# Performance work log

Measured on AMD Instinct MI355X. Metric: run time of the kernel, lower is better.

Reference implementation:

```python
import jax, jax.numpy as jnp
import numpy as np

SHIFTS = [1, 3, 5, 7]
C = 16  # in_channels // 4
# -1 neighbor offsets for tmp1..tmp8 (dy, dx) in units of the dilation
OFFSETS = [(-1, -1), (-1, 0), (-1, 1), (0, 1), (1, 1), (1, 0), (1, -1), (0, -1)]


def setup_inputs() -> dict:
    key = jax.random.key(0)
    ks = jax.random.split(key, 32)
    d = {}
    d['cen'] = jax.random.normal(ks[0], (8, 64, 256, 256), jnp.float32)
    d['mas'] = jax.random.normal(ks[1], (8, 1, 256, 256), jnp.float32)
    d['in_conv_w'] = jax.random.normal(ks[2], (16, 64), jnp.float32) * 0.1
    d['in_conv_b'] = jax.random.normal(ks[3], (16,), jnp.float32) * 0.1
    for i, s in enumerate(SHIFTS):
        d[f'dw_w{s}'] = jax.random.normal(ks[4 + 2 * i], (16, 1, s, s), jnp.float32) * 0.1
        d[f'dw_b{s}'] = jax.random.normal(ks[5 + 2 * i], (16,), jnp.float32) * 0.1
    d['l1_w'] = jax.random.normal(ks[12], (4, 16, 4), jnp.float32) * 0.1
    d['l1_b'] = jax.random.normal(ks[13], (4, 16), jnp.float32) * 0.1
    d['l2_w'] = jax.random.normal(ks[14], (4, 16, 8), jnp.float32) * 0.1
    d['l2_b'] = jax.random.normal(ks[15], (4, 16), jnp.float32) * 0.1
    d['base_w'] = jax.random.normal(ks[16], (16, 4), jnp.float32) * 0.1
    d['bn_scale'] = jnp.ones((16,), jnp.float32)
    d['bn_bias'] = jnp.zeros((16,), jnp.float32)
    d['final_w'] = jax.random.normal(ks[17], (1, 16), jnp.float32) * 0.1
    d['final_b'] = jax.random.normal(ks[18], (1,), jnp.float32) * 0.1
    return d


def _dw_conv(x, w, b, pad):
    # depthwise conv, groups == channels
    y = jax.lax.conv_general_dilated(
        x, w, window_strides=(1, 1), padding=[(pad, pad), (pad, pad)],
        dimension_numbers=('NCHW', 'OIHW', 'NCHW'), feature_group_count=x.shape[1])
    return y + b[None, :, None, None]


def _shifted(x, dy, dx, d):
    # zero-padded shift: out(y,x) = in(y+dy, x+dx)
    H, W = x.shape[2], x.shape[3]
    p = jnp.pad(x, ((0, 0), (0, 0), (d, d), (d, d)))
    return p[:, :, d + dy:d + dy + H, d + dx:d + dx + W]


def _circ_shift(x, dw_w, dw_b, w1, b1, w2, b2, shift):
    x = _dw_conv(x, dw_w, dw_b, shift // 2)
    # tmp_k = x - x shifted by the k-th neighbor offset (dilation = shift)
    T = [x - _shifted(x, dy * shift, dx * shift, shift) for dy, dx in OFFSETS]
    # paired sums: S[k] = tmp_{k+1} + tmp_{k+5} (S repeats with period 4)
    S = [T[k] + T[k + 4] for k in range(4)]
    outs = []
    for k in range(8):  # fixed small structural loop
        feats = jnp.stack([S[(k + 1) % 4], S[(k + 3) % 4], S[(k + 2) % 4],
                           2.0 * T[(k + 4) % 8]], axis=2)  # (B,C,4,H,W)
        # grouped 1x1 conv (groups=C, 4C->C) == per-channel contraction over feature axis
        o = jnp.einsum('bcfhw,cf->bchw', feats, w1) + b1[None, :, None, None]
        outs.append(o * T[k])
    O = jnp.sort(jnp.stack(outs, axis=2), axis=2)  # (B,C,8,H,W) sorted over branch axis
    return jnp.einsum('bcfhw,cf->bchw', O, w2) + b2[None, :, None, None]


def reference(cen, mas, in_conv_w, in_conv_b, dw_w1, dw_b1, dw_w3, dw_b3,
              dw_w5, dw_b5, dw_w7, dw_b7, l1_w, l1_b, l2_w, l2_b,
              base_w, bn_scale, bn_bias, final_w, final_b):
    # in_conv: 1x1, in_channels -> C
    x = jnp.einsum('bihw,oi->bohw', cen, in_conv_w) + in_conv_b[None, :, None, None]
    dws = [(dw_w1, dw_b1), (dw_w3, dw_b3), (dw_w5, dw_b5), (dw_w7, dw_b7)]
    branches = [
        _circ_shift(x, dws[i][0], dws[i][1], l1_w[i], l1_b[i], l2_w[i], l2_b[i], SHIFTS[i])
        for i in range(len(SHIFTS))
    ]
    A = jnp.sort(jnp.stack(branches, axis=2), axis=2)  # (B,C,4,H,W)
    # out_conv: grouped 1x1 BaseConv (conv no-bias + BN(affine) + SiLU), then 1x1 -> 1, sigmoid
    y = jnp.einsum('bcfhw,cf->bchw', A, base_w)
    y = jax.nn.silu(y * bn_scale[None, :, None, None] + bn_bias[None, :, None, None])
    y = jnp.einsum('bchw,oc->bohw', y, final_w) + final_b[None, :, None, None]
    return jax.nn.sigmoid(y)
```

## Files before the change

kernel.cpp:

```cpp
#include <hip/hip_runtime.h>
#include <hip/hip_fp16.h>
#include <math.h>

#define HW 65536

typedef float v2f __attribute__((ext_vector_type(2), aligned(8)));
typedef _Float16 h2 __attribute__((ext_vector_type(2)));

__device__ __forceinline__ h2 uh(unsigned u) { return __builtin_bit_cast(h2, u); }
__device__ __forceinline__ unsigned hu(h2 v) { return __builtin_bit_cast(unsigned, v); }

#define CEH(a, b) { h2 _t = __builtin_elementwise_min(a, b); \
                    b = __builtin_elementwise_max(a, b); a = _t; }

__device__ __forceinline__ void sort8_h2(h2* v) {
    CEH(v[0], v[1]); CEH(v[2], v[3]); CEH(v[4], v[5]); CEH(v[6], v[7]);
    CEH(v[0], v[2]); CEH(v[1], v[3]); CEH(v[4], v[6]); CEH(v[5], v[7]);
    CEH(v[1], v[2]); CEH(v[5], v[6]); CEH(v[0], v[4]); CEH(v[3], v[7]);
    CEH(v[1], v[5]); CEH(v[2], v[6]);
    CEH(v[1], v[4]); CEH(v[3], v[6]);
    CEH(v[2], v[4]); CEH(v[3], v[5]);
    CEH(v[3], v[4]);
}
__device__ __forceinline__ void sort4_h2(h2* v) {
    CEH(v[0], v[1]); CEH(v[2], v[3]); CEH(v[0], v[2]); CEH(v[1], v[3]); CEH(v[1], v[2]);
}

__global__ __launch_bounds__(256) void k_pack(const float* __restrict__ l1w,
                                              const float* __restrict__ l1b,
                                              const float* __restrict__ l2w,
                                              const float* __restrict__ l2b,
                                              const float* __restrict__ bw,
                                              const float* __restrict__ dw_w1,
                                              const float* __restrict__ dw_b1,
                                              const float* __restrict__ dw_w3,
                                              const float* __restrict__ dw_b3,
                                              const float* __restrict__ dw_w5,
                                              const float* __restrict__ dw_b5,
                                              const float* __restrict__ dw_w7,
                                              const float* __restrict__ dw_b7,
                                              unsigned* __restrict__ wtab) {
    for (int t = threadIdx.x; t < 3584; t += 256) {
        float v = 0.f;
        if (t < 1024) {
            int c = t >> 6, i = (t >> 4) & 3, j = t & 15;
            if (j < 3)        v = l1w[i * 64 + c * 4 + j];
            else if (j == 3)  v = 2.f * l1w[i * 64 + c * 4 + 3];
            else if (j == 4)  v = l1b[i * 16 + c];
            else if (j < 13)  v = l2w[i * 128 + c * 8 + (j - 5)];
            else if (j == 13) v = l2b[i * 16 + c];
        } else if (t < 1088) {
            v = bw[t - 1024];
        } else if (t >= 2048) {
            int c = (t - 2048) / 96, j = (t - 2048) - c * 96;
            if (j < 49)       v = dw_w7[c * 49 + j];
            else if (j < 74)  v = dw_w5[c * 25 + (j - 49)];
            else if (j < 83)  v = dw_w3[c * 9 + (j - 74)];
            else if (j == 83) v = dw_w1[c];
            else if (j == 84) v = dw_b1[c];
            else if (j == 85) v = dw_b3[c];
            else if (j == 86) v = dw_b5[c];
            else if (j == 87) v = dw_b7[c];
        }
        unsigned hs = (unsigned)__half_as_ushort(__float2half(v));
        wtab[t] = hs * 0x10001u;
    }
}

__global__ __launch_bounds__(256, 4) void k_inconv(const float* __restrict__ cen,
                                                   const float* __restrict__ w,
                                                   const float* __restrict__ bias,
                                                   __half* __restrict__ xh) {
    __shared__ float wl[1040];
    int tid = threadIdx.x;
    for (int t = tid; t < 1024; t += 256) wl[t] = w[(t & 15) * 64 + (t >> 4)];
    if (tid < 16) wl[1024 + tid] = bias[tid];
    __syncthreads();

    int q  = blockIdx.x * 256 + tid;
    int b_ = q >> 14;
    int hw = (q & 16383) * 4;
    const float* src = cen + (size_t)(b_ * 64) * HW + hw;

    float4 acc[16];
#pragma unroll
    for (int o = 0; o < 16; o++) { float bv = wl[1024 + o]; acc[o] = make_float4(bv, bv, bv, bv); }

#pragma unroll 4
    for (int i = 0; i < 64; i++) {
        float4 xv = *(const float4*)(src + (size_t)i * HW);
        const float4* wq = (const float4*)&wl[i * 16];
#pragma unroll
        for (int g = 0; g < 4; g++) {
            float4 f = wq[g];
            acc[g * 4 + 0].x += xv.x * f.x; acc[g * 4 + 0].y += xv.y * f.x;
            acc[g * 4 + 0].z += xv.z * f.x; acc[g * 4 + 0].w += xv.w * f.x;
            acc[g * 4 + 1].x += xv.x * f.y; acc[g * 4 + 1].y += xv.y * f.y;
            acc[g * 4 + 1].z += xv.z * f.y; acc[g * 4 + 1].w += xv.w * f.y;
            acc[g * 4 + 2].x += xv.x * f.z; acc[g * 4 + 2].y += xv.y * f.z;
            acc[g * 4 + 2].z += xv.z * f.z; acc[g * 4 + 2].w += xv.w * f.z;
            acc[g * 4 + 3].x += xv.x * f.w; acc[g * 4 + 3].y += xv.y * f.w;
            acc[g * 4 + 3].z += xv.z * f.w; acc[g * 4 + 3].w += xv.w * f.w;
        }
    }
    __half* dst = xh + (size_t)(b_ * 16) * HW + hw;
#pragma unroll
    for (int o = 0; o < 16; o++) {
        uint2 pk;
        pk.x = __builtin_bit_cast(unsigned, __floats2half2_rn(acc[o].x, acc[o].y));
        pk.y = __builtin_bit_cast(unsigned, __floats2half2_rn(acc[o].z, acc[o].w));
        *(uint2*)(dst + (size_t)o * HW) = pk;
    }
}

__global__ __launch_bounds__(512, 4) void k_fused(const __half* __restrict__ xh,
    const unsigned* __restrict__ wtab,
    const float* __restrict__ bns, const float* __restrict__ bnb,
    __half* __restrict__ y16) {

    const int by  = blockIdx.y;
    const int c   = by & 15;
    const int ty0 = (blockIdx.x >> 3) * 32;
    const int tx0 = (blockIdx.x & 7) * 32;
    const int tid = threadIdx.x;

    __shared__ unsigned lxh[52 * 27];
    __shared__ __align__(16) unsigned convt[4 * 46 * 24];

    {
        const unsigned* xp32 = (const unsigned*)(xh + (size_t)by * HW);
        for (int t = tid; t < 52 * 26; t += 512) {
            int r = t / 26, j = t - r * 26;
            int gy = ty0 - 10 + r, gp = tx0 - 10 + 2 * j;
            unsigned v = 0;
            if ((unsigned)gy < 256u && (unsigned)gp < 256u)
                v = xp32[(gy << 7) + (gp >> 1)];
            lxh[r * 27 + j] = v;
        }
    }
    __syncthreads();

    {
        const unsigned* dwc = wtab + 2048 + c * 96;
        for (int u = tid; u < 46 * 23; u += 512) {
            int row = u / 23;
            int d0  = u - row * 23;
            int pc0 = d0 * 2;
            h2 acc7 = {0, 0}, acc5 = {0, 0}, acc3 = {0, 0}, acc1 = {0, 0};
#pragma unroll
            for (int a = 0; a < 7; a++) {
                const unsigned* rp = lxh + (row + a) * 27 + d0;
                unsigned q0 = rp[0], q1 = rp[1], q2 = rp[2], q3 = rp[3], q4 = rp[4];
                unsigned p1u = (q0 >> 16) | (q1 << 16);
                unsigned p3u = (q1 >> 16) | (q2 << 16);
                unsigned p5u = (q2 >> 16) | (q3 << 16);
                unsigned p7u = (q3 >> 16) | (q4 << 16);
                h2 P[8] = {uh(q0), uh(p1u), uh(q1), uh(p3u),
                           uh(q2), uh(p5u), uh(q3), uh(p7u)};
#pragma unroll
                for (int b = 0; b < 7; b++)
                    acc7 = P[b] * uh(dwc[a * 7 + b]) + acc7;
                if (a >= 1 && a <= 5) {
#pragma unroll
                    for (int b = 0; b < 5; b++)
                        acc5 = P[1 + b] * uh(dwc[49 + (a - 1) * 5 + b]) + acc5;
                }
                if (a >= 2 && a <= 4) {
#pragma unroll
                    for (int b = 0; b < 3; b++)
                        acc3 = P[2 + b] * uh(dwc[74 + (a - 2) * 3 + b]) + acc3;
                }
                if (a == 3)
                    acc1 = P[3] * uh(dwc[83]);
            }
            int iy = ty0 - 7 + row, ix = tx0 - 7 + pc0;
            bool rin = (unsigned)iy < 256u;
            unsigned msk = (rin && (unsigned)ix < 256u ? 0x0000FFFFu : 0u)
                         | (rin && (unsigned)(ix + 1) < 256u ? 0xFFFF0000u : 0u);
            int o = row * 24 + d0;
            convt[o]        = hu(acc1 + uh(dwc[84])) & msk;
            convt[o + 1104] = hu(acc3 + uh(dwc[85])) & msk;
            convt[o + 2208] = hu(acc5 + uh(dwc[86])) & msk;
            convt[o + 3312] = hu(acc7 + uh(dwc[87])) & msk;
        }
    }
    __syncthreads();

    const int py  = tid >> 4;
    const int pxp = tid & 15;

    h2 bh[4];
#pragma unroll
    for (int i = 0; i < 4; i++) {
        const int s = 1 + 2 * i;
        const unsigned* pl = convt + i * 1104;
        const int q    = pxp + (7 - s) / 2;
        const int topb = (py + 7 - s) * 24 + q;
        const int midb = (py + 7) * 24 + q;
        const int botb = (py + 7 + s) * 24 + q;

        unsigned tt[8], tm[8], tb[8];
#pragma unroll
        for (int k = 0; k <= s; k++) {
            tt[k] = pl[topb + k];
            tm[k] = pl[midb + k];
            tb[k] = pl[botb + k];
        }
        const int m = s >> 1;
        h2 n0  = uh(tt[0]);
        h2 n1  = uh((tt[m] >> 16) | (tt[m + 1] << 16));
        h2 n2  = uh(tt[s]);
        h2 n7  = uh(tm[0]);
        h2 ctr = uh((tm[m] >> 16) | (tm[m + 1] << 16));
        h2 n3  = uh(tm[s]);
        h2 n6  = uh(tb[0]);
        h2 n5  = uh((tb[m] >> 16) | (tb[m + 1] << 16));
        h2 n4  = uh(tb[s]);

        h2 T[8];
        T[0] = ctr - n0; T[1] = ctr - n1; T[2] = ctr - n2; T[3] = ctr - n3;
        T[4] = ctr - n4; T[5] = ctr - n5; T[6] = ctr - n6; T[7] = ctr - n7;
        h2 S[4];
#pragma unroll
        for (int k = 0; k < 4; k++) S[k] = T[k] + T[k + 4];

        const unsigned* wt = wtab + ((c << 2) + i) * 16;
        h2 w10 = uh(wt[0]), w11 = uh(wt[1]), w12 = uh(wt[2]);
        h2 w13x2 = uh(wt[3]), bb1 = uh(wt[4]);

        h2 R[4];
#pragma unroll
        for (int mm = 0; mm < 4; mm++) {
            h2 r = S[(mm + 2) & 3] * w12 + bb1;
            r = S[(mm + 3) & 3] * w11 + r;
            r = S[(mm + 1) & 3] * w10 + r;
            R[mm] = r;
        }
        h2 h8[8];
#pragma unroll
        for (int k = 0; k < 8; k++)
            h8[k] = (T[(k + 4) & 7] * w13x2 + R[k & 3]) * T[k];
        sort8_h2(h8);

        h2 acc = uh(wt[13]);
#pragma unroll
        for (int k = 0; k < 8; k++) acc += h8[k] * uh(wt[5 + k]);
        bh[i] = acc;
    }
    sort4_h2(bh);
    h2 yv = bh[0] * uh(wtab[1024 + (c << 2)]);
#pragma unroll
    for (int k = 1; k < 4; k++) yv = bh[k] * uh(wtab[1024 + (c << 2) + k]) + yv;

    const float bsc = bns[c], bbi = bnb[c];
    float zx = fmaf((float)yv.x, bsc, bbi);
    float zy = fmaf((float)yv.y, bsc, bbi);
    float sx = zx / (1.f + __expf(-zx));
    float sy = zy / (1.f + __expf(-zy));
    *(__half2*)&y16[(size_t)by * HW + (ty0 + py) * 256 + tx0 + 2 * pxp] =
        __floats2half2_rn(sx, sy);
}

__global__ __launch_bounds__(256) void k_final(const __half* __restrict__ y16,
                                               const float* __restrict__ fw,
                                               const float* __restrict__ fb,
                                               float* __restrict__ out) {
    long t  = (long)blockIdx.x * 256 + threadIdx.x;
    long p0 = t * 2;
    int  b  = (int)(p0 >> 16);
    int  hw = (int)(p0 & 65535);

    float accx = fb[0], accy = fb[0];
#pragma unroll
    for (int cc = 0; cc < 16; cc++) {
        __half2 h = *(const __half2*)(y16 + (size_t)(b * 16 + cc) * HW + hw);
        float2 v = __half22float2(h);
        float wv = fw[cc];
        accx = fmaf(v.x, wv, accx);
        accy = fmaf(v.y, wv, accy);
    }
    float2 r;
    r.x = 1.f / (1.f + __expf(-accx));
    r.y = 1.f / (1.f + __expf(-accy));
    *(float2*)(out + p0) = r;
}

extern "C" void kernel_launch(void* const* d_in, const int* in_sizes, int n_in,
                              void* d_out, int out_size, void* d_ws, size_t ws_size,
                              hipStream_t stream) {
    (void)in_sizes; (void)n_in; (void)out_size; (void)ws_size;
    const float* cen   = (const float*)d_in[0];
    const float* in_w  = (const float*)d_in[2];
    const float* in_b  = (const float*)d_in[3];
    const float* dw_w1 = (const float*)d_in[4];
    const float* dw_b1 = (const float*)d_in[5];
    const float* dw_w3 = (const float*)d_in[6];
    const float* dw_b3 = (const float*)d_in[7];
    const float* dw_w5 = (const float*)d_in[8];
    const float* dw_b5 = (const float*)d_in[9];
    const float* dw_w7 = (const float*)d_in[10];
    const float* dw_b7 = (const float*)d_in[11];
    const float* l1w   = (const float*)d_in[12];
    const float* l1b   = (const float*)d_in[13];
    const float* l2w   = (const float*)d_in[14];
    const float* l2b   = (const float*)d_in[15];
    const float* bw    = (const float*)d_in[16];
    const float* bns   = (const float*)d_in[17];
    const float* bnb   = (const float*)d_in[18];
    const float* fw    = (const float*)d_in[19];
    const float* fb    = (const float*)d_in[20];

    __half*   xh   = (__half*)d_ws;
    unsigned* wtab = (unsigned*)((char*)d_ws + (size_t)16777216);
    __half*   y16  = (__half*)((char*)d_ws + (size_t)16777216 + 16384);
    float*    out  = (float*)d_out;

    k_pack<<<1, 256, 0, stream>>>(l1w, l1b, l2w, l2b, bw,
                                  dw_w1, dw_b1, dw_w3, dw_b3,
                                  dw_w5, dw_b5, dw_w7, dw_b7, wtab);
    k_inconv<<<512, 256, 0, stream>>>(cen, in_w, in_b, xh);
    k_fused<<<dim3(64, 128), 512, 0, stream>>>(xh, wtab, bns, bnb, y16);
    k_final<<<1024, 256, 0, stream>>>(y16, fw, fb, out);
}
```

Measured before the change: 359.1 us.

## Enlarge fused tile to 64x64 with 1024 threads; narrow inconv per-thread width

The fused kernel moves from 32x32 to 64x64 spatial tiles with 1024 threads, each thread computing two output rows. This cuts the halo overhead of the staged input and the depthwise-conv intermediates relative to useful output. Shared-memory strides change to 43 and 40 words, and the conv loop no longer loads an unused fifth word. The in_conv kernel now handles 2 pixels per thread instead of 4 and launches twice as many blocks for more parallelism. The cost is higher LDS use per block (about 64 KB here), which may limit occupancy, plus fewer fused blocks overall.

```diff
diff --git a/kernel.cpp b/kernel.cpp
--- a/kernel.cpp
+++ b/kernel.cpp
@@ -77,86 +77,79 @@
     if (tid < 16) wl[1024 + tid] = bias[tid];
     __syncthreads();
 
-    int q  = blockIdx.x * 256 + tid;
-    int b_ = q >> 14;
-    int hw = (q & 16383) * 4;
+    int pr = blockIdx.x * 256 + tid;
+    int b_ = pr >> 15;
+    int hw = (pr & 32767) * 2;
     const float* src = cen + (size_t)(b_ * 64) * HW + hw;
 
-    float4 acc[16];
-#pragma unroll
-    for (int o = 0; o < 16; o++) { float bv = wl[1024 + o]; acc[o] = make_float4(bv, bv, bv, bv); }
-
-#pragma unroll 4
+    v2f acc[16];
+#pragma unroll
+    for (int o = 0; o < 16; o++) { float bv = wl[1024 + o]; v2f t = {bv, bv}; acc[o] = t; }
+
+#pragma unroll 8
     for (int i = 0; i < 64; i++) {
-        float4 xv = *(const float4*)(src + (size_t)i * HW);
+        v2f xv = *(const v2f*)(src + (size_t)i * HW);
         const float4* wq = (const float4*)&wl[i * 16];
 #pragma unroll
         for (int g = 0; g < 4; g++) {
             float4 f = wq[g];
-            acc[g * 4 + 0].x += xv.x * f.x; acc[g * 4 + 0].y += xv.y * f.x;
-            acc[g * 4 + 0].z += xv.z * f.x; acc[g * 4 + 0].w += xv.w * f.x;
-            acc[g * 4 + 1].x += xv.x * f.y; acc[g * 4 + 1].y += xv.y * f.y;
-            acc[g * 4 + 1].z += xv.z * f.y; acc[g * 4 + 1].w += xv.w * f.y;
-            acc[g * 4 + 2].x += xv.x * f.z; acc[g * 4 + 2].y += xv.y * f.z;
-            acc[g * 4 + 2].z += xv.z * f.z; acc[g * 4 + 2].w += xv.w * f.z;
-            acc[g * 4 + 3].x += xv.x * f.w; acc[g * 4 + 3].y += xv.y * f.w;
-            acc[g * 4 + 3].z += xv.z * f.w; acc[g * 4 + 3].w += xv.w * f.w;
+            acc[g * 4 + 0] += xv * f.x;
+            acc[g * 4 + 1] += xv * f.y;
+            acc[g * 4 + 2] += xv * f.z;
+            acc[g * 4 + 3] += xv * f.w;
         }
     }
     __half* dst = xh + (size_t)(b_ * 16) * HW + hw;
 #pragma unroll
-    for (int o = 0; o < 16; o++) {
-        uint2 pk;
-        pk.x = __builtin_bit_cast(unsigned, __floats2half2_rn(acc[o].x, acc[o].y));
-        pk.y = __builtin_bit_cast(unsigned, __floats2half2_rn(acc[o].z, acc[o].w));
-        *(uint2*)(dst + (size_t)o * HW) = pk;
-    }
-}
-
-__global__ __launch_bounds__(512, 4) void k_fused(const __half* __restrict__ xh,
+    for (int o = 0; o < 16; o++)
+        *(__half2*)(dst + (size_t)o * HW) = __floats2half2_rn(acc[o].x, acc[o].y);
+}
+
+#define LXS 43
+#define CTS 40
+#define CTP (78 * CTS)
+__global__ __launch_bounds__(1024, 4) void k_fused(const __half* __restrict__ xh,
     const unsigned* __restrict__ wtab,
     const float* __restrict__ bns, const float* __restrict__ bnb,
     __half* __restrict__ y16) {
 
     const int by  = blockIdx.y;
     const int c   = by & 15;
-    const int ty0 = (blockIdx.x >> 3) * 32;
-    const int tx0 = (blockIdx.x & 7) * 32;
+    const int ty0 = (blockIdx.x >> 2) * 64;
+    const int tx0 = (blockIdx.x & 3) * 64;
     const int tid = threadIdx.x;
 
-    __shared__ unsigned lxh[52 * 27];
-    __shared__ __align__(16) unsigned convt[4 * 46 * 24];
+    __shared__ unsigned lxh[84 * LXS];
+    __shared__ unsigned convt[4 * CTP];
 
     {
         const unsigned* xp32 = (const unsigned*)(xh + (size_t)by * HW);
-        for (int t = tid; t < 52 * 26; t += 512) {
-            int r = t / 26, j = t - r * 26;
+        for (int t = tid; t < 84 * 42; t += 1024) {
+            int r = t / 42, j = t - r * 42;
             int gy = ty0 - 10 + r, gp = tx0 - 10 + 2 * j;
             unsigned v = 0;
             if ((unsigned)gy < 256u && (unsigned)gp < 256u)
                 v = xp32[(gy << 7) + (gp >> 1)];
-            lxh[r * 27 + j] = v;
+            lxh[r * LXS + j] = v;
         }
     }
     __syncthreads();
 
     {
         const unsigned* dwc = wtab + 2048 + c * 96;
-        for (int u = tid; u < 46 * 23; u += 512) {
-            int row = u / 23;
-            int d0  = u - row * 23;
-            int pc0 = d0 * 2;
+        for (int u = tid; u < 78 * 39; u += 1024) {
+            int row = u / 39;
+            int d0  = u - row * 39;
             h2 acc7 = {0, 0}, acc5 = {0, 0}, acc3 = {0, 0}, acc1 = {0, 0};
 #pragma unroll
             for (int a = 0; a < 7; a++) {
-                const unsigned* rp = lxh + (row + a) * 27 + d0;
-                unsigned q0 = rp[0], q1 = rp[1], q2 = rp[2], q3 = rp[3], q4 = rp[4];
+                const unsigned* rp = lxh + (row + a) * LXS + d0;
+                unsigned q0 = rp[0], q1 = rp[1], q2 = rp[2], q3 = rp[3];
                 unsigned p1u = (q0 >> 16) | (q1 << 16);
                 unsigned p3u = (q1 >> 16) | (q2 << 16);
                 unsigned p5u = (q2 >> 16) | (q3 << 16);
-                unsigned p7u = (q3 >> 16) | (q4 << 16);
-                h2 P[8] = {uh(q0), uh(p1u), uh(q1), uh(p3u),
-                           uh(q2), uh(p5u), uh(q3), uh(p7u)};
+                h2 P[7] = {uh(q0), uh(p1u), uh(q1), uh(p3u),
+                           uh(q2), uh(p5u), uh(q3)};
 #pragma unroll
                 for (int b = 0; b < 7; b++)
                     acc7 = P[b] * uh(dwc[a * 7 + b]) + acc7;
@@ -173,92 +166,97 @@
                 if (a == 3)
                     acc1 = P[3] * uh(dwc[83]);
             }
-            int iy = ty0 - 7 + row, ix = tx0 - 7 + pc0;
+            int iy = ty0 - 7 + row, ix = tx0 - 7 + 2 * d0;
             bool rin = (unsigned)iy < 256u;
             unsigned msk = (rin && (unsigned)ix < 256u ? 0x0000FFFFu : 0u)
                          | (rin && (unsigned)(ix + 1) < 256u ? 0xFFFF0000u : 0u);
-            int o = row * 24 + d0;
-            convt[o]        = hu(acc1 + uh(dwc[84])) & msk;
-            convt[o + 1104] = hu(acc3 + uh(dwc[85])) & msk;
-            convt[o + 2208] = hu(acc5 + uh(dwc[86])) & msk;
-            convt[o + 3312] = hu(acc7 + uh(dwc[87])) & msk;
+            int o = row * CTS + d0;
+            convt[o]           = hu(acc1 + uh(dwc[84])) & msk;
+            convt[o + CTP]     = hu(acc3 + uh(dwc[85])) & msk;
+            convt[o + 2 * CTP] = hu(acc5 + uh(dwc[86])) & msk;
+            convt[o + 3 * CTP] = hu(acc7 + uh(dwc[87])) & msk;
         }
     }
     __syncthreads();
 
-    const int py  = tid >> 4;
-    const int pxp = tid & 15;
-
-    h2 bh[4];
-#pragma unroll
-    for (int i = 0; i < 4; i++) {
-        const int s = 1 + 2 * i;
-        const unsigned* pl = convt + i * 1104;
-        const int q    = pxp + (7 - s) / 2;
-        const int topb = (py + 7 - s) * 24 + q;
-        const int midb = (py + 7) * 24 + q;
-        const int botb = (py + 7 + s) * 24 + q;
-
-        unsigned tt[8], tm[8], tb[8];
-#pragma unroll
-        for (int k = 0; k <= s; k++) {
-            tt[k] = pl[topb + k];
-            tm[k] = pl[midb + k];
-            tb[k] = pl[botb + k];
-        }
-        const int m = s >> 1;
-        h2 n0  = uh(tt[0]);
-        h2 n1  = uh((tt[m] >> 16) | (tt[m + 1] << 16));
-        h2 n2  = uh(tt[s]);
-        h2 n7  = uh(tm[0]);
-        h2 ctr = uh((tm[m] >> 16) | (tm[m + 1] << 16));
-        h2 n3  = uh(tm[s]);
-        h2 n6  = uh(tb[0]);
-        h2 n5  = uh((tb[m] >> 16) | (tb[m + 1] << 16));
-        h2 n4  = uh(tb[s]);
-
-        h2 T[8];
-        T[0] = ctr - n0; T[1] = ctr - n1; T[2] = ctr - n2; T[3] = ctr - n3;
-        T[4] = ctr - n4; T[5] = ctr - n5; T[6] = ctr - n6; T[7] = ctr - n7;
-        h2 S[4];
-#pragma unroll
-        for (int k = 0; k < 4; k++) S[k] = T[k] + T[k + 4];
-
-        const unsigned* wt = wtab + ((c << 2) + i) * 16;
-        h2 w10 = uh(wt[0]), w11 = uh(wt[1]), w12 = uh(wt[2]);
-        h2 w13x2 = uh(wt[3]), bb1 = uh(wt[4]);
-
-        h2 R[4];
-#pragma unroll
-        for (int mm = 0; mm < 4; mm++) {
-            h2 r = S[(mm + 2) & 3] * w12 + bb1;
-            r = S[(mm + 3) & 3] * w11 + r;
-            r = S[(mm + 1) & 3] * w10 + r;
-            R[mm] = r;
-        }
-        h2 h8[8];
-#pragma unroll
-        for (int k = 0; k < 8; k++)
-            h8[k] = (T[(k + 4) & 7] * w13x2 + R[k & 3]) * T[k];
-        sort8_h2(h8);
-
-        h2 acc = uh(wt[13]);
-#pragma unroll
-        for (int k = 0; k < 8; k++) acc += h8[k] * uh(wt[5 + k]);
-        bh[i] = acc;
-    }
-    sort4_h2(bh);
-    h2 yv = bh[0] * uh(wtab[1024 + (c << 2)]);
-#pragma unroll
-    for (int k = 1; k < 4; k++) yv = bh[k] * uh(wtab[1024 + (c << 2) + k]) + yv;
-
-    const float bsc = bns[c], bbi = bnb[c];
-    float zx = fmaf((float)yv.x, bsc, bbi);
-    float zy = fmaf((float)yv.y, bsc, bbi);
-    float sx = zx / (1.f + __expf(-zx));
-    float sy = zy / (1.f + __expf(-zy));
-    *(__half2*)&y16[(size_t)by * HW + (ty0 + py) * 256 + tx0 + 2 * pxp] =
-        __floats2half2_rn(sx, sy);
+    const int py  = tid >> 5;
+    const int pxp = tid & 31;
+
+#pragma unroll
+    for (int rr = 0; rr < 2; rr++) {
+        const int R = py + (rr << 5);
+
+        h2 bh[4];
+#pragma unroll
+        for (int i = 0; i < 4; i++) {
+            const int s = 1 + 2 * i;
+            const unsigned* pl = convt + i * CTP;
+            const int q    = pxp + (7 - s) / 2;
+            const int topb = (R + 7 - s) * CTS + q;
+            const int midb = (R + 7) * CTS + q;
+            const int botb = (R + 7 + s) * CTS + q;
+
+            unsigned tt[8], tm[8], tb[8];
+#pragma unroll
+            for (int k = 0; k <= s; k++) {
+                tt[k] = pl[topb + k];
+                tm[k] = pl[midb + k];
+                tb[k] = pl[botb + k];
+            }
+            const int m = s >> 1;
+            h2 n0  = uh(tt[0]);
+            h2 n1  = uh((tt[m] >> 16) | (tt[m + 1] << 16));
+            h2 n2  = uh(tt[s]);
+            h2 n7  = uh(tm[0]);
+            h2 ctr = uh((tm[m] >> 16) | (tm[m + 1] << 16));
+            h2 n3  = uh(tm[s]);
+            h2 n6  = uh(tb[0]);
+            h2 n5  = uh((tb[m] >> 16) | (tb[m + 1] << 16));
+            h2 n4  = uh(tb[s]);
+
+            h2 T[8];
+            T[0] = ctr - n0; T[1] = ctr - n1; T[2] = ctr - n2; T[3] = ctr - n3;
+            T[4] = ctr - n4; T[5] = ctr - n5; T[6] = ctr - n6; T[7] = ctr - n7;
+            h2 S[4];
+#pragma unroll
+            for (int k = 0; k < 4; k++) S[k] = T[k] + T[k + 4];
+
+            const unsigned* wt = wtab + ((c << 2) + i) * 16;
+            h2 w10 = uh(wt[0]), w11 = uh(wt[1]), w12 = uh(wt[2]);
+            h2 w13x2 = uh(wt[3]), bb1 = uh(wt[4]);
+
+            h2 R4[4];
+#pragma unroll
+            for (int mm = 0; mm < 4; mm++) {
+                h2 r = S[(mm + 2) & 3] * w12 + bb1;
+                r = S[(mm + 3) & 3] * w11 + r;
+                r = S[(mm + 1) & 3] * w10 + r;
+                R4[mm] = r;
+            }
+            h2 h8[8];
+#pragma unroll
+            for (int k = 0; k < 8; k++)
+                h8[k] = (T[(k + 4) & 7] * w13x2 + R4[k & 3]) * T[k];
+            sort8_h2(h8);
+
+            h2 acc = uh(wt[13]);
+#pragma unroll
+            for (int k = 0; k < 8; k++) acc += h8[k] * uh(wt[5 + k]);
+            bh[i] = acc;
+        }
+        sort4_h2(bh);
+        h2 yv = bh[0] * uh(wtab[1024 + (c << 2)]);
+#pragma unroll
+        for (int k = 1; k < 4; k++) yv = bh[k] * uh(wtab[1024 + (c << 2) + k]) + yv;
+
+        const float bsc = bns[c], bbi = bnb[c];
+        float zx = fmaf((float)yv.x, bsc, bbi);
+        float zy = fmaf((float)yv.y, bsc, bbi);
+        float sx = zx / (1.f + __expf(-zx));
+        float sy = zy / (1.f + __expf(-zy));
+        *(__half2*)&y16[(size_t)by * HW + (ty0 + R) * 256 + tx0 + 2 * pxp] =
+            __floats2half2_rn(sx, sy);
+    }
 }
 
 __global__ __launch_bounds__(256) void k_final(const __half* __restrict__ y16,
@@ -318,7 +316,7 @@
     k_pack<<<1, 256, 0, stream>>>(l1w, l1b, l2w, l2b, bw,
                                   dw_w1, dw_b1, dw_w3, dw_b3,
                                   dw_w5, dw_b5, dw_w7, dw_b7, wtab);
-    k_inconv<<<512, 256, 0, stream>>>(cen, in_w, in_b, xh);
-    k_fused<<<dim3(64, 128), 512, 0, stream>>>(xh, wtab, bns, bnb, y16);
+    k_inconv<<<1024, 256, 0, stream>>>(cen, in_w, in_b, xh);
+    k_fused<<<dim3(16, 128), 1024, 0, stream>>>(xh, wtab, bns, bnb, y16);
     k_final<<<1024, 256, 0, stream>>>(y16, fw, fb, out);
 }
```

Result: faster. 344.7 us (-4.0%).
